# Performance work log

Hardware: AMD Instinct MI355X
Metric: run time of the kernel (lower is better)

The kernel has to match this reference:

```python
import jax, jax.numpy as jnp
import numpy as np

NUM_GROUPS = 32
EPS = 1e-6


def group_norm(x, scale, bias):
    # x: (b, c, t, h, w)
    b, c, t, h, w = x.shape
    xg = x.reshape(b, NUM_GROUPS, c // NUM_GROUPS, t, h, w)
    mean = jnp.mean(xg, axis=(2, 3, 4, 5), keepdims=True)
    var = jnp.var(xg, axis=(2, 3, 4, 5), keepdims=True)
    xg = (xg - mean) * jax.lax.rsqrt(var + EPS)
    xn = xg.reshape(b, c, t, h, w)
    return xn * scale[None, :, None, None, None] + bias[None, :, None, None, None]


def conv1x1(x, w, bvec):
    # 1x1x1 Conv3d == per-position linear over channels
    return jnp.einsum('oc,bcthw->bothw', w, x) + bvec[None, :, None, None, None]


def setup_inputs() -> dict:
    key = jax.random.key(0)
    ks = jax.random.split(key, 11)
    b, c, t, h, w = 2, 256, 4, 32, 32
    x = jax.random.normal(ks[0], (b, c, t, h, w), dtype=jnp.float32)
    s = 1.0 / np.sqrt(c)
    return {
        'x': x,
        'gn_scale': jnp.ones((c,), jnp.float32),
        'gn_bias': jnp.zeros((c,), jnp.float32),
        'wq': jax.random.normal(ks[1], (c, c), jnp.float32) * s,
        'bq': jax.random.normal(ks[2], (c,), jnp.float32) * 0.01,
        'wk': jax.random.normal(ks[3], (c, c), jnp.float32) * s,
        'bk': jax.random.normal(ks[4], (c,), jnp.float32) * 0.01,
        'wv': jax.random.normal(ks[5], (c, c), jnp.float32) * s,
        'bv': jax.random.normal(ks[6], (c,), jnp.float32) * 0.01,
        'wp': jax.random.normal(ks[7], (c, c), jnp.float32) * s,
        'bp': jax.random.normal(ks[8], (c,), jnp.float32) * 0.01,
    }


def reference(x, gn_scale, gn_bias, wq, bq, wk, bk, wv, bv, wp, bp):
    b, c, t, h, w = x.shape
    n = t * h * w
    h_ = group_norm(x, gn_scale, gn_bias)
    q = conv1x1(h_, wq, bq).reshape(b, c, n)  # (b, c, n)
    k = conv1x1(h_, wk, bk).reshape(b, c, n)
    v = conv1x1(h_, wv, bv).reshape(b, c, n)
    scale = jnp.asarray(int(c) ** (-0.5), x.dtype)
    # attn[b, i, j] = sum_c q[b,c,i] k[b,c,j]
    attn = jnp.einsum('bci,bcj->bij', q, k) * scale
    attn = jax.nn.softmax(attn, axis=2)
    # A[b, c, i] = sum_j v[b,c,j] attn[b,i,j]
    A = jnp.einsum('bcj,bij->bci', v, attn).reshape(b, c, t, h, w)
    A = conv1x1(A, wp, bp)
    return x + A
```

## Files before the change

### kernel.cpp

```cpp
#include <hip/hip_runtime.h>
#include <hip/hip_bf16.h>
#include <math.h>

#define BB 2
#define CC 256
#define GG 32
#define NN 4096
#define EPSF 1e-6f
#define JSPLIT 8
#define JBLK (NN / JSPLIT)
#define CH 32
#define NT (JBLK / CH)
#define QTILE 128
#define LOG2E 1.4426950408889634f

typedef _Float16 f16x8 __attribute__((ext_vector_type(8)));
typedef float f32x4 __attribute__((ext_vector_type(4)));
typedef float f32x16 __attribute__((ext_vector_type(16)));

static __device__ __forceinline__ unsigned short f2h_bits(float f) {
    _Float16 h = (_Float16)f;
    return __builtin_bit_cast(unsigned short, h);
}
static __device__ __forceinline__ unsigned pkh2(float a, float b) {
    return __builtin_bit_cast(unsigned, __builtin_amdgcn_cvt_pkrtz(a, b));
}
static __device__ __forceinline__ void gload16(const void* g, void* l) {
    __builtin_amdgcn_global_load_lds(
        (const __attribute__((address_space(1))) void*)g,
        (__attribute__((address_space(3))) void*)l, 16, 0, 0);
}

__global__ __launch_bounds__(256) void prep_w16_kernel(
    const float* __restrict__ wq, const float* __restrict__ wk,
    const float* __restrict__ wv, const float* __restrict__ wp,
    unsigned short* __restrict__ w16)
{
    int m = blockIdx.y;
    const float* src = (m == 0) ? wq : (m == 1) ? wk : (m == 2) ? wv : wp;
    float scale = (m == 0) ? 0.0625f * LOG2E : 1.0f;
    int idx = blockIdx.x * 256 + threadIdx.x;
    float4 v = ((const float4*)src)[idx];
    union { _Float16 h[4]; uint2 u; } pk;
    pk.h[0] = (_Float16)(v.x * scale);
    pk.h[1] = (_Float16)(v.y * scale);
    pk.h[2] = (_Float16)(v.z * scale);
    pk.h[3] = (_Float16)(v.w * scale);
    *(uint2*)(w16 + (size_t)m * CC * CC + (size_t)idx * 4) = pk.u;
}

__global__ __launch_bounds__(256) void gn_part_kernel(
    const float* __restrict__ x, float2* __restrict__ part)
{
    int g = blockIdx.x, p = blockIdx.y, b = blockIdx.z;
    const float* base = x + ((size_t)b * CC + (size_t)g * 8) * NN + (size_t)p * 8192;
    int t = threadIdx.x;
    float s = 0.f, ss = 0.f;
    for (int idx = t; idx < 2048; idx += 256) {
        float4 v4 = ((const float4*)base)[idx];
        s  += v4.x + v4.y + v4.z + v4.w;
        ss += v4.x*v4.x + v4.y*v4.y + v4.z*v4.z + v4.w*v4.w;
    }
    for (int off = 32; off; off >>= 1) {
        s  += __shfl_down(s,  off);
        ss += __shfl_down(ss, off);
    }
    __shared__ float red[8];
    int wid = t >> 6;
    if ((t & 63) == 0) { red[wid*2] = s; red[wid*2+1] = ss; }
    __syncthreads();
    if (t == 0) {
        part[(b*GG + g)*4 + p] = make_float2(red[0]+red[2]+red[4]+red[6],
                                             red[1]+red[3]+red[5]+red[7]);
    }
}

__global__ __launch_bounds__(256) void proj_qkv_kernel(
    const float* __restrict__ x, const float* __restrict__ sc,
    const float* __restrict__ bi, const float2* __restrict__ part,
    const unsigned short* __restrict__ w16,
    const float* __restrict__ bq, const float* __restrict__ bk,
    const float* __restrict__ bv,
    unsigned short* __restrict__ qT, unsigned short* __restrict__ kT,
    unsigned short* __restrict__ vC)
{
    int b  = blockIdx.y;
    int i0 = blockIdx.x * 32;
    int t  = threadIdx.x;
    __shared__ unsigned short htile[32 * 256];
    __shared__ float s_mean[GG], s_rstd[GG], s_sc[CC], s_bi[CC];
    if (t < GG) {
        float2 p0 = part[(b*GG + t)*4 + 0];
        float2 p1 = part[(b*GG + t)*4 + 1];
        float2 p2 = part[(b*GG + t)*4 + 2];
        float2 p3 = part[(b*GG + t)*4 + 3];
        float S  = p0.x + p1.x + p2.x + p3.x;
        float SS = p0.y + p1.y + p2.y + p3.y;
        float mean = S / 32768.f;
        float var  = SS / 32768.f - mean * mean;
        s_mean[t] = mean;
        s_rstd[t] = rsqrtf(var + EPSF);
    }
    s_sc[t] = sc[t];
    s_bi[t] = bi[t];
    __syncthreads();

    char* hw = (char*)htile;
    int nq = (t & 7) * 4;
    int cq = (t >> 3) * 4;
    #pragma unroll
    for (int k = 0; k < 2; k++) {
        int c0 = cq + k * 128;
        float4 xr[4];
        float aa[4], dd[4];
        #pragma unroll
        for (int e = 0; e < 4; e++) {
            int c = c0 + e;
            xr[e] = *(const float4*)(x + ((size_t)b*CC + c)*NN + i0 + nq);
            aa[e] = s_rstd[c >> 3] * s_sc[c];
            dd[e] = s_bi[c] - s_mean[c >> 3] * aa[e];
        }
        #pragma unroll
        for (int j = 0; j < 4; j++) {
            int row = nq + j;
            union { _Float16 h[4]; uint2 u; } pk;
            pk.h[0] = (_Float16)(((const float*)&xr[0])[j] * aa[0] + dd[0]);
            pk.h[1] = (_Float16)(((const float*)&xr[1])[j] * aa[1] + dd[1]);
            pk.h[2] = (_Float16)(((const float*)&xr[2])[j] * aa[2] + dd[2]);
            pk.h[3] = (_Float16)(((const float*)&xr[3])[j] * aa[3] + dd[3]);
            int off = row*512 + (((c0 >> 3) ^ (row & 7)) << 4) + (c0 & 7) * 2;
            *(uint2*)(hw + off) = pk.u;
        }
    }
    __syncthreads();

    int lane = t & 63, w = t >> 6;
    int col = lane & 15, grp = lane >> 4;
    const char* hr = (const char*)htile;

    #pragma unroll
    for (int p = 0; p < 2; p++) {
        const unsigned short* wgt = w16 + (size_t)p * CC * CC;
        const float* bias = p ? bk : bq;
        unsigned short* outp = (p ? kT : qT) + (size_t)b * NN * CC;
        float osc = p ? 1.0f : 0.0625f * LOG2E;
        #pragma unroll
        for (int ot = 0; ot < 4; ot++) {
            int ow = ot * 64 + w * 16;
            f32x4 acc[2];
            acc[0] = (f32x4){0.f,0.f,0.f,0.f};
            acc[1] = (f32x4){0.f,0.f,0.f,0.f};
            #pragma unroll
            for (int ck = 0; ck < 8; ck++) {
                f16x8 af = *(const f16x8*)(wgt + (size_t)(ow + col)*CC + ck*32 + grp*8);
                #pragma unroll
                for (int it = 0; it < 2; it++) {
                    int row = it*16 + col;
                    f16x8 bf = *(const f16x8*)(hr + row*512 + (((ck*4 + grp) ^ (row & 7)) << 4));
                    acc[it] = __builtin_amdgcn_mfma_f32_16x16x32_f16(af, bf, acc[it], 0, 0, 0);
                }
            }
            int obase = ow + grp * 4;
            float b0 = bias[obase]*osc, b1 = bias[obase+1]*osc,
                  b2 = bias[obase+2]*osc, b3 = bias[obase+3]*osc;
            #pragma unroll
            for (int it = 0; it < 2; it++) {
                int i = i0 + it*16 + col;
                union { _Float16 h[4]; uint2 u; } pk;
                pk.h[0] = (_Float16)(acc[it][0] + b0);
                pk.h[1] = (_Float16)(acc[it][1] + b1);
                pk.h[2] = (_Float16)(acc[it][2] + b2);
                pk.h[3] = (_Float16)(acc[it][3] + b3);
                *(uint2*)(outp + (size_t)i*CC + obase) = pk.u;
            }
        }
    }
    {
        const unsigned short* wgt = w16 + (size_t)2 * CC * CC;
        unsigned short* outp = vC + (size_t)b * CC * NN;
        int ibase = (w & 1) * 16;
        #pragma unroll
        for (int gg = 0; gg < 2; gg++) {
            int og = (w >> 1) * 2 + gg;
            f32x4 acc[4];
            #pragma unroll
            for (int ot = 0; ot < 4; ot++) acc[ot] = (f32x4){0.f,0.f,0.f,0.f};
            #pragma unroll
            for (int ck = 0; ck < 8; ck++) {
                int row = ibase + col;
                f16x8 af = *(const f16x8*)(hr + row*512 + (((ck*4 + grp) ^ (row & 7)) << 4));
                #pragma unroll
                for (int ot = 0; ot < 4; ot++) {
                    f16x8 bf = *(const f16x8*)(wgt + (size_t)(og*64 + ot*16 + col)*CC + ck*32 + grp*8);
                    acc[ot] = __builtin_amdgcn_mfma_f32_16x16x32_f16(af, bf, acc[ot], 0, 0, 0);
                }
            }
            int iw = i0 + ibase + grp * 4;
            #pragma unroll
            for (int ot = 0; ot < 4; ot++) {
                int o = og*64 + ot*16 + col;
                float bo = bv[o];
                union { _Float16 h[4]; uint2 u; } pk;
                pk.h[0] = (_Float16)(acc[ot][0] + bo);
                pk.h[1] = (_Float16)(acc[ot][1] + bo);
                pk.h[2] = (_Float16)(acc[ot][2] + bo);
                pk.h[3] = (_Float16)(acc[ot][3] + bo);
                *(uint2*)(outp + (size_t)o*NN + iw) = pk.u;
            }
        }
    }
}

#define STAGE_K(tt, bb) do { int _j = jlo + (tt)*CH; _Pragma("unroll") \
    for (int e = 0; e < 4; e++) gload16(kb + (size_t)_j*CC + koff[e], &bufK[bb][(4*w + e)*512]); } while (0)
#define STAGE_V(tt, bb) do { int _j = jlo + (tt)*CH; _Pragma("unroll") \
    for (int e = 0; e < 4; e++) gload16(vb + voff[e] + _j, &bufV[bb][(4*w + e)*512]); } while (0)

__global__ __launch_bounds__(256, 2) void attn_kernel(
    const unsigned short* __restrict__ qT,
    const unsigned short* __restrict__ kT,
    const unsigned short* __restrict__ vC,
    unsigned short* __restrict__ pO,
    float2* __restrict__ ml)
{
    int qt = blockIdx.x, s = blockIdx.y, b = blockIdx.z;
    int tid = threadIdx.x, w = tid >> 6, lane = tid & 63;
    int l31 = lane & 31, hi = lane >> 5;
    int col = lane & 15, grp = lane >> 4;
    int q0 = qt * QTILE + w * 32;
    int jlo = s * JBLK;

    __shared__ __align__(16) unsigned short bufK[2][8192];
    __shared__ __align__(16) unsigned short bufV[2][8192];
    __shared__ __align__(16) unsigned short plds[4 * 1280];

    const unsigned short* qb = qT + (size_t)b * NN * CC;
    const unsigned short* kb = kT + (size_t)b * NN * CC;
    const unsigned short* vb = vC + (size_t)b * CC * NN;

    f16x8 qf[16];
    #pragma unroll
    for (int ck = 0; ck < 16; ck++)
        qf[ck] = *(const f16x8*)(qb + (size_t)(q0 + l31)*CC + ck*16 + hi*8);

    int koff[4], voff[4];
    #pragma unroll
    for (int e = 0; e < 4; e++) {
        int blk = (4*w + e)*64 + lane;
        int kj = blk >> 5, kcb = blk & 31;
        koff[e] = kj*CC + ((kcb ^ (kj & 7)) * 8);
        int vc = blk >> 2, vcb = blk & 3;
        voff[e] = vc*NN + ((vcb ^ ((vc >> 1) & 3)) * 8);
    }
    int kru = l31 * 512;
    int kx  = l31 & 7;
    int vrb = col*64 + ((grp ^ ((col >> 1) & 3)) << 4);
    char* pw  = (char*)plds + w*2560 + l31*80 + 8*hi;
    const char* prd = (const char*)plds + w*2560;

    f32x4 O0[16], O1[16];
    #pragma unroll
    for (int ct = 0; ct < 16; ct++) {
        O0[ct] = (f32x4){0.f,0.f,0.f,0.f};
        O1[ct] = (f32x4){0.f,0.f,0.f,0.f};
    }
    float m = -1e30f, l = 0.f;

    STAGE_K(0, 0);
    STAGE_V(0, 0);
    __syncthreads();

    for (int t = 0; t < NT; t++) {
        int cur = t & 1;
        if (t + 1 < NT) {
            STAGE_K(t + 1, cur ^ 1);
            STAGE_V(t + 1, cur ^ 1);
        }
        const char* kbase = (const char*)&bufK[cur][0];
        const char* vbase = (const char*)&bufV[cur][0];

        f32x16 S;
        #pragma unroll
        for (int r = 0; r < 16; r++) S[r] = 0.f;
        __builtin_amdgcn_s_setprio(1);
        #pragma unroll
        for (int ck = 0; ck < 16; ck++) {
            f16x8 kf = *(const f16x8*)(kbase + kru + ((((ck*2) | hi) ^ kx) << 4));
            S = __builtin_amdgcn_mfma_f32_32x32x16_f16(kf, qf[ck], S, 0, 0, 0);
        }
        __builtin_amdgcn_s_setprio(0);

        float x0 = fmaxf(fmaxf(S[0], S[1]), fmaxf(S[2], S[3]));
        float x1 = fmaxf(fmaxf(S[4], S[5]), fmaxf(S[6], S[7]));
        float x2 = fmaxf(fmaxf(S[8], S[9]), fmaxf(S[10], S[11]));
        float x3 = fmaxf(fmaxf(S[12], S[13]), fmaxf(S[14], S[15]));
        float mh = fmaxf(fmaxf(x0, x1), fmaxf(x2, x3));
        float mx = fmaxf(mh, __shfl_xor(mh, 32));

        if (!__all(mx <= m + 8.f)) {
            float mn = fmaxf(m, mx);
            float f = exp2f(m - mn);
            m = mn;
            l *= f;
            float fq0 = __shfl(f, col);
            float fq1 = __shfl(f, 16 + col);
            #pragma unroll
            for (int ct = 0; ct < 16; ct++) { O0[ct] *= fq0; O1[ct] *= fq1; }
        }

        #pragma unroll
        for (int r = 0; r < 16; r++) S[r] = exp2f(S[r] - m);
        float ps = (((S[0]+S[1]) + (S[2]+S[3])) + ((S[4]+S[5]) + (S[6]+S[7])))
                 + (((S[8]+S[9]) + (S[10]+S[11])) + ((S[12]+S[13]) + (S[14]+S[15])));
        l += ps + __shfl_xor(ps, 32);

        {
            unsigned* pr = (unsigned*)pw;
            pr[0]  = pkh2(S[0],  S[1]);   pr[1]  = pkh2(S[2],  S[3]);
            pr[4]  = pkh2(S[4],  S[5]);   pr[5]  = pkh2(S[6],  S[7]);
            pr[8]  = pkh2(S[8],  S[9]);   pr[9]  = pkh2(S[10], S[11]);
            pr[12] = pkh2(S[12], S[13]);  pr[13] = pkh2(S[14], S[15]);
        }
        asm volatile("s_waitcnt lgkmcnt(0)" ::: "memory");
        __builtin_amdgcn_sched_barrier(0);

        f16x8 y0 = *(const f16x8*)(prd + col*80 + grp*16);
        f16x8 y1 = *(const f16x8*)(prd + (16 + col)*80 + grp*16);
        __builtin_amdgcn_s_setprio(1);
        #pragma unroll
        for (int ct = 0; ct < 16; ct++) {
            f16x8 xf = *(const f16x8*)(vbase + ct*1024 + vrb);
            O0[ct] = __builtin_amdgcn_mfma_f32_16x16x32_f16(xf, y0, O0[ct], 0, 0, 0);
            O1[ct] = __builtin_amdgcn_mfma_f32_16x16x32_f16(xf, y1, O1[ct], 0, 0, 0);
        }
        __builtin_amdgcn_s_setprio(0);
        __syncthreads();
    }

    float inv = 1.f / l;
    float iq0 = __shfl(inv, col);
    float iq1 = __shfl(inv, 16 + col);
    unsigned short* po = pO + ((size_t)(s*BB + b)*NN + q0) * CC;
    #pragma unroll
    for (int ct = 0; ct < 16; ct++) {
        int c = ct*16 + grp*4;
        *(unsigned*)(po + (size_t)col*CC + c)            = pkh2(O0[ct][0]*iq0, O0[ct][1]*iq0);
        *(unsigned*)(po + (size_t)col*CC + c + 2)        = pkh2(O0[ct][2]*iq0, O0[ct][3]*iq0);
        *(unsigned*)(po + (size_t)(16 + col)*CC + c)     = pkh2(O1[ct][0]*iq1, O1[ct][1]*iq1);
        *(unsigned*)(po + (size_t)(16 + col)*CC + c + 2) = pkh2(O1[ct][2]*iq1, O1[ct][3]*iq1);
    }
    if (lane < 32)
        ml[(size_t)(s*BB + b)*NN + q0 + lane] = make_float2(m, l);
}

__global__ __launch_bounds__(256) void attn_merge_kernel(
    const unsigned short* __restrict__ pO, const float2* __restrict__ ml,
    unsigned short* __restrict__ aT)
{
    int t = threadIdx.x;
    int qrow = blockIdx.x * 16 + (t >> 4);
    int c0 = (t & 15) * 16;
    float M = -1e30f;
    float m8[JSPLIT], l8[JSPLIT];
    #pragma unroll
    for (int s = 0; s < JSPLIT; s++) {
        float2 v = ml[(size_t)s*BB*NN + qrow];
        m8[s] = v.x; l8[s] = v.y;
        M = fmaxf(M, v.x);
    }
    float W = 0.f, wt[JSPLIT];
    #pragma unroll
    for (int s = 0; s < JSPLIT; s++) { wt[s] = l8[s] * exp2f(m8[s] - M); W += wt[s]; }
    float iW = 1.f / W;
    float acc[16];
    #pragma unroll
    for (int e = 0; e < 16; e++) acc[e] = 0.f;
    #pragma unroll
    for (int s = 0; s < JSPLIT; s++) {
        const unsigned short* p = pO + ((size_t)s*BB*NN + qrow)*CC + c0;
        f16x8 a0 = *(const f16x8*)p;
        f16x8 a1 = *(const f16x8*)(p + 8);
        float ws = wt[s] * iW;
        #pragma unroll
        for (int e = 0; e < 8; e++) {
            acc[e]     += ws * (float)a0[e];
            acc[e + 8] += ws * (float)a1[e];
        }
    }
    union { _Float16 h[8]; uint4 u; } o0, o1;
    #pragma unroll
    for (int e = 0; e < 8; e++) { o0.h[e] = (_Float16)acc[e]; o1.h[e] = (_Float16)acc[e+8]; }
    unsigned short* dst = aT + (size_t)qrow*CC + c0;
    *(uint4*)dst = o0.u;
    *(uint4*)(dst + 8) = o1.u;
}

__global__ __launch_bounds__(256) void proj_out_kernel(
    const unsigned short* __restrict__ aT,
    const unsigned short* __restrict__ wp16, const float* __restrict__ bp,
    const float* __restrict__ x, float* __restrict__ out)
{
    int b = blockIdx.z;
    int i0 = blockIdx.x * 64, o0 = blockIdx.y * 64;
    int lane = threadIdx.x & 63, wid = threadIdx.x >> 6;
    int col = lane & 15, grp = lane >> 4;
    int ibase = i0 + wid * 16;
    const unsigned short* ab = aT + (size_t)b*NN*CC;
    f32x4 acc[4];
    for (int ot = 0; ot < 4; ot++) acc[ot] = (f32x4){0.f,0.f,0.f,0.f};
    for (int ck = 0; ck < 8; ck++) {
        f16x8 af = *(const f16x8*)(ab + (size_t)(ibase + col)*CC + ck*32 + grp*8);
        for (int ot = 0; ot < 4; ot++) {
            f16x8 bf = *(const f16x8*)(wp16 + (size_t)(o0 + ot*16 + col)*CC + ck*32 + grp*8);
            acc[ot] = __builtin_amdgcn_mfma_f32_16x16x32_f16(af, bf, acc[ot], 0, 0, 0);
        }
    }
    int iw = ibase + grp * 4;
    for (int ot = 0; ot < 4; ot++) {
        int o = o0 + ot*16 + col;
        float bo = bp[o];
        size_t base = (size_t)b*CC*NN + (size_t)o*NN + iw;
        float4 x4 = *(const float4*)(x + base);
        float4 r;
        r.x = x4.x + acc[ot][0] + bo;
        r.y = x4.y + acc[ot][1] + bo;
        r.z = x4.z + acc[ot][2] + bo;
        r.w = x4.w + acc[ot][3] + bo;
        *(float4*)(out + base) = r;
    }
}

extern "C" void kernel_launch(void* const* d_in, const int* in_sizes, int n_in,
                              void* d_out, int out_size, void* d_ws, size_t ws_size,
                              hipStream_t stream) {
    const float* x  = (const float*)d_in[0];
    const float* gs = (const float*)d_in[1];
    const float* gb = (const float*)d_in[2];
    const float* wq = (const float*)d_in[3];
    const float* bq = (const float*)d_in[4];
    const float* wk = (const float*)d_in[5];
    const float* bk = (const float*)d_in[6];
    const float* wv = (const float*)d_in[7];
    const float* bv = (const float*)d_in[8];
    const float* wp = (const float*)d_in[9];
    const float* bp = (const float*)d_in[10];
    float* out = (float*)d_out;

    char* ws = (char*)d_ws;
    const size_t sz = (size_t)BB * NN * CC * sizeof(unsigned short);
    unsigned short* qT  = (unsigned short*)(ws + sz);
    unsigned short* kT  = (unsigned short*)(ws + 2*sz);
    unsigned short* vC  = (unsigned short*)(ws + 3*sz);
    unsigned short* aT  = (unsigned short*)(ws + 4*sz);
    unsigned short* w16 = (unsigned short*)(ws + 5*sz);
    float2* part        = (float2*)(ws + 5*sz + 512*1024);
    float2* ml          = (float2*)(ws + 5*sz + 768*1024);
    unsigned short* pO  = (unsigned short*)(ws + 5*sz + 1280*1024);

    prep_w16_kernel<<<dim3(CC*CC/4/256, 4), 256, 0, stream>>>(wq, wk, wv, wp, w16);
    gn_part_kernel<<<dim3(GG, 4, BB), 256, 0, stream>>>(x, part);
    proj_qkv_kernel<<<dim3(NN/32, BB), 256, 0, stream>>>(x, gs, gb, part, w16,
                                                         bq, bk, bv, qT, kT, vC);
    attn_kernel<<<dim3(NN/QTILE, JSPLIT, BB), 256, 0, stream>>>(qT, kT, vC, pO, ml);
    attn_merge_kernel<<<dim3(BB*NN/16), 256, 0, stream>>>(pO, ml, aT);
    proj_out_kernel<<<dim3(NN/64, CC/64, BB), 256, 0, stream>>>(aT, w16 + 3*CC*CC, bp, x, out);
}
```

Before: 125.0 us.

## Read K and V tiles directly from global memory instead of LDS staging

Removes the double-buffered global-to-LDS staging of K and V tiles and the per-iteration block barrier, so each wave loads its K and V MFMA fragments straight from global memory (relying on L1/L2 for reuse across waves). This cuts LDS usage, which may allow higher occupancy, and removes the synchronisation. In exchange, every wave issues redundant global loads for the same tiles, with strided V accesses and no prefetch overlap, which risks exposing memory latency inside the MFMA loops.

Result: slower. 196.7 us (+57.4%).

```diff
diff --git a/kernel.cpp b/kernel.cpp
--- a/kernel.cpp
+++ b/kernel.cpp
@@ -24,11 +24,6 @@
 }
 static __device__ __forceinline__ unsigned pkh2(float a, float b) {
     return __builtin_bit_cast(unsigned, __builtin_amdgcn_cvt_pkrtz(a, b));
-}
-static __device__ __forceinline__ void gload16(const void* g, void* l) {
-    __builtin_amdgcn_global_load_lds(
-        (const __attribute__((address_space(1))) void*)g,
-        (__attribute__((address_space(3))) void*)l, 16, 0, 0);
 }
 
 __global__ __launch_bounds__(256) void prep_w16_kernel(
@@ -211,11 +206,6 @@
     }
 }
 
-#define STAGE_K(tt, bb) do { int _j = jlo + (tt)*CH; _Pragma("unroll") \
-    for (int e = 0; e < 4; e++) gload16(kb + (size_t)_j*CC + koff[e], &bufK[bb][(4*w + e)*512]); } while (0)
-#define STAGE_V(tt, bb) do { int _j = jlo + (tt)*CH; _Pragma("unroll") \
-    for (int e = 0; e < 4; e++) gload16(vb + voff[e] + _j, &bufV[bb][(4*w + e)*512]); } while (0)
-
 __global__ __launch_bounds__(256, 2) void attn_kernel(
     const unsigned short* __restrict__ qT,
     const unsigned short* __restrict__ kT,
@@ -230,8 +220,6 @@
     int q0 = qt * QTILE + w * 32;
     int jlo = s * JBLK;
 
-    __shared__ __align__(16) unsigned short bufK[2][8192];
-    __shared__ __align__(16) unsigned short bufV[2][8192];
     __shared__ __align__(16) unsigned short plds[4 * 1280];
 
     const unsigned short* qb = qT + (size_t)b * NN * CC;
@@ -243,18 +231,9 @@
     for (int ck = 0; ck < 16; ck++)
         qf[ck] = *(const f16x8*)(qb + (size_t)(q0 + l31)*CC + ck*16 + hi*8);
 
-    int koff[4], voff[4];
-    #pragma unroll
-    for (int e = 0; e < 4; e++) {
-        int blk = (4*w + e)*64 + lane;
-        int kj = blk >> 5, kcb = blk & 31;
-        koff[e] = kj*CC + ((kcb ^ (kj & 7)) * 8);
-        int vc = blk >> 2, vcb = blk & 3;
-        voff[e] = vc*NN + ((vcb ^ ((vc >> 1) & 3)) * 8);
-    }
-    int kru = l31 * 512;
-    int kx  = l31 & 7;
-    int vrb = col*64 + ((grp ^ ((col >> 1) & 3)) << 4);
+    const unsigned short* krow = kb + (size_t)(jlo + l31)*CC + hi*8;
+    const unsigned short* vrow = vb + (size_t)col*NN + jlo + grp*8;
+
     char* pw  = (char*)plds + w*2560 + l31*80 + 8*hi;
     const char* prd = (const char*)plds + w*2560;
 
@@ -266,26 +245,14 @@
     }
     float m = -1e30f, l = 0.f;
 
-    STAGE_K(0, 0);
-    STAGE_V(0, 0);
-    __syncthreads();
-
     for (int t = 0; t < NT; t++) {
-        int cur = t & 1;
-        if (t + 1 < NT) {
-            STAGE_K(t + 1, cur ^ 1);
-            STAGE_V(t + 1, cur ^ 1);
-        }
-        const char* kbase = (const char*)&bufK[cur][0];
-        const char* vbase = (const char*)&bufV[cur][0];
-
         f32x16 S;
         #pragma unroll
         for (int r = 0; r < 16; r++) S[r] = 0.f;
         __builtin_amdgcn_s_setprio(1);
         #pragma unroll
         for (int ck = 0; ck < 16; ck++) {
-            f16x8 kf = *(const f16x8*)(kbase + kru + ((((ck*2) | hi) ^ kx) << 4));
+            f16x8 kf = *(const f16x8*)(krow + ck*16);
             S = __builtin_amdgcn_mfma_f32_32x32x16_f16(kf, qf[ck], S, 0, 0, 0);
         }
         __builtin_amdgcn_s_setprio(0);
@@ -329,12 +296,14 @@
         __builtin_amdgcn_s_setprio(1);
         #pragma unroll
         for (int ct = 0; ct < 16; ct++) {
-            f16x8 xf = *(const f16x8*)(vbase + ct*1024 + vrb);
+            f16x8 xf = *(const f16x8*)(vrow + (size_t)(ct*16)*NN);
             O0[ct] = __builtin_amdgcn_mfma_f32_16x16x32_f16(xf, y0, O0[ct], 0, 0, 0);
             O1[ct] = __builtin_amdgcn_mfma_f32_16x16x32_f16(xf, y1, O1[ct], 0, 0, 0);
         }
         __builtin_amdgcn_s_setprio(0);
-        __syncthreads();
+
+        krow += (size_t)CH * CC;
+        vrow += CH;
     }
 
     float inv = 1.f / l;
```

## Fuse split-softmax merge into output projection and combine prep kernels

Applied to the files above, without the earlier changes.

Merges the weight fp16 conversion and group-norm partial-sum kernels into one launch by block-id dispatch. Fuses the attention split merge into the output projection: each block merges the JSPLIT partial outputs for 32 query rows into a swizzled LDS tile, then runs MFMA against Wp and adds the residual. This removes two launches and the aT round trip through global memory, at the cost of fewer, larger blocks in the final stage.

Result: faster. 116.9 us (median of 2 runs) (-6.4%).

```diff
diff --git a/kernel.cpp b/kernel.cpp
--- a/kernel.cpp
+++ b/kernel.cpp
@@ -12,6 +12,7 @@
 #define CH 32
 #define NT (JBLK / CH)
 #define QTILE 128
+#define ITILE 32
 #define LOG2E 1.4426950408889634f
 
 typedef _Float16 f16x8 __attribute__((ext_vector_type(8)));
@@ -31,47 +32,48 @@
         (__attribute__((address_space(3))) void*)l, 16, 0, 0);
 }
 
-__global__ __launch_bounds__(256) void prep_w16_kernel(
+__global__ __launch_bounds__(256) void prep_gn_kernel(
     const float* __restrict__ wq, const float* __restrict__ wk,
     const float* __restrict__ wv, const float* __restrict__ wp,
-    unsigned short* __restrict__ w16)
-{
-    int m = blockIdx.y;
-    const float* src = (m == 0) ? wq : (m == 1) ? wk : (m == 2) ? wv : wp;
-    float scale = (m == 0) ? 0.0625f * LOG2E : 1.0f;
-    int idx = blockIdx.x * 256 + threadIdx.x;
-    float4 v = ((const float4*)src)[idx];
-    union { _Float16 h[4]; uint2 u; } pk;
-    pk.h[0] = (_Float16)(v.x * scale);
-    pk.h[1] = (_Float16)(v.y * scale);
-    pk.h[2] = (_Float16)(v.z * scale);
-    pk.h[3] = (_Float16)(v.w * scale);
-    *(uint2*)(w16 + (size_t)m * CC * CC + (size_t)idx * 4) = pk.u;
-}
-
-__global__ __launch_bounds__(256) void gn_part_kernel(
+    unsigned short* __restrict__ w16,
     const float* __restrict__ x, float2* __restrict__ part)
 {
-    int g = blockIdx.x, p = blockIdx.y, b = blockIdx.z;
-    const float* base = x + ((size_t)b * CC + (size_t)g * 8) * NN + (size_t)p * 8192;
-    int t = threadIdx.x;
-    float s = 0.f, ss = 0.f;
-    for (int idx = t; idx < 2048; idx += 256) {
-        float4 v4 = ((const float4*)base)[idx];
-        s  += v4.x + v4.y + v4.z + v4.w;
-        ss += v4.x*v4.x + v4.y*v4.y + v4.z*v4.z + v4.w*v4.w;
-    }
-    for (int off = 32; off; off >>= 1) {
-        s  += __shfl_down(s,  off);
-        ss += __shfl_down(ss, off);
-    }
     __shared__ float red[8];
-    int wid = t >> 6;
-    if ((t & 63) == 0) { red[wid*2] = s; red[wid*2+1] = ss; }
-    __syncthreads();
-    if (t == 0) {
-        part[(b*GG + g)*4 + p] = make_float2(red[0]+red[2]+red[4]+red[6],
-                                             red[1]+red[3]+red[5]+red[7]);
+    int id = blockIdx.x;
+    int t  = threadIdx.x;
+    if (id < 256) {
+        int m = id >> 6;
+        const float* src = (m == 0) ? wq : (m == 1) ? wk : (m == 2) ? wv : wp;
+        float scale = (m == 0) ? 0.0625f * LOG2E : 1.0f;
+        int idx = (id & 63) * 256 + t;
+        float4 v = ((const float4*)src)[idx];
+        union { _Float16 h[4]; uint2 u; } pk;
+        pk.h[0] = (_Float16)(v.x * scale);
+        pk.h[1] = (_Float16)(v.y * scale);
+        pk.h[2] = (_Float16)(v.z * scale);
+        pk.h[3] = (_Float16)(v.w * scale);
+        *(uint2*)(w16 + (size_t)m * CC * CC + (size_t)idx * 4) = pk.u;
+    } else {
+        int rem = id - 256;
+        int g = rem & 31, p = (rem >> 5) & 3, b = rem >> 7;
+        const float* base = x + ((size_t)b * CC + (size_t)g * 8) * NN + (size_t)p * 8192;
+        float s = 0.f, ss = 0.f;
+        for (int idx = t; idx < 2048; idx += 256) {
+            float4 v4 = ((const float4*)base)[idx];
+            s  += v4.x + v4.y + v4.z + v4.w;
+            ss += v4.x*v4.x + v4.y*v4.y + v4.z*v4.z + v4.w*v4.w;
+        }
+        for (int off = 32; off; off >>= 1) {
+            s  += __shfl_down(s,  off);
+            ss += __shfl_down(ss, off);
+        }
+        int wid = t >> 6;
+        if ((t & 63) == 0) { red[wid*2] = s; red[wid*2+1] = ss; }
+        __syncthreads();
+        if (t == 0) {
+            part[(b*GG + g)*4 + p] = make_float2(red[0]+red[2]+red[4]+red[6],
+                                                 red[1]+red[3]+red[5]+red[7]);
+        }
     }
 }
 
@@ -353,80 +355,96 @@
         ml[(size_t)(s*BB + b)*NN + q0 + lane] = make_float2(m, l);
 }
 
-__global__ __launch_bounds__(256) void attn_merge_kernel(
+__global__ __launch_bounds__(256, 2) void proj_out_merge_kernel(
     const unsigned short* __restrict__ pO, const float2* __restrict__ ml,
-    unsigned short* __restrict__ aT)
-{
-    int t = threadIdx.x;
-    int qrow = blockIdx.x * 16 + (t >> 4);
-    int c0 = (t & 15) * 16;
-    float M = -1e30f;
-    float m8[JSPLIT], l8[JSPLIT];
-    #pragma unroll
-    for (int s = 0; s < JSPLIT; s++) {
-        float2 v = ml[(size_t)s*BB*NN + qrow];
-        m8[s] = v.x; l8[s] = v.y;
-        M = fmaxf(M, v.x);
-    }
-    float W = 0.f, wt[JSPLIT];
-    #pragma unroll
-    for (int s = 0; s < JSPLIT; s++) { wt[s] = l8[s] * exp2f(m8[s] - M); W += wt[s]; }
-    float iW = 1.f / W;
-    float acc[16];
-    #pragma unroll
-    for (int e = 0; e < 16; e++) acc[e] = 0.f;
-    #pragma unroll
-    for (int s = 0; s < JSPLIT; s++) {
-        const unsigned short* p = pO + ((size_t)s*BB*NN + qrow)*CC + c0;
-        f16x8 a0 = *(const f16x8*)p;
-        f16x8 a1 = *(const f16x8*)(p + 8);
-        float ws = wt[s] * iW;
-        #pragma unroll
-        for (int e = 0; e < 8; e++) {
-            acc[e]     += ws * (float)a0[e];
-            acc[e + 8] += ws * (float)a1[e];
-        }
-    }
-    union { _Float16 h[8]; uint4 u; } o0, o1;
-    #pragma unroll
-    for (int e = 0; e < 8; e++) { o0.h[e] = (_Float16)acc[e]; o1.h[e] = (_Float16)acc[e+8]; }
-    unsigned short* dst = aT + (size_t)qrow*CC + c0;
-    *(uint4*)dst = o0.u;
-    *(uint4*)(dst + 8) = o1.u;
-}
-
-__global__ __launch_bounds__(256) void proj_out_kernel(
-    const unsigned short* __restrict__ aT,
     const unsigned short* __restrict__ wp16, const float* __restrict__ bp,
     const float* __restrict__ x, float* __restrict__ out)
 {
-    int b = blockIdx.z;
-    int i0 = blockIdx.x * 64, o0 = blockIdx.y * 64;
-    int lane = threadIdx.x & 63, wid = threadIdx.x >> 6;
+    int b  = blockIdx.y;
+    int i0 = blockIdx.x * ITILE;
+    int t  = threadIdx.x;
+    __shared__ __align__(16) unsigned short htile[ITILE * 256];
+
+    {
+        int row  = t >> 3;
+        int cseg = (t & 7) * 32;
+        size_t qrow = (size_t)b * NN + i0 + row;
+        float M = -1e30f;
+        float m8[JSPLIT], l8[JSPLIT];
+        #pragma unroll
+        for (int s = 0; s < JSPLIT; s++) {
+            float2 v = ml[(size_t)s*BB*NN + qrow];
+            m8[s] = v.x; l8[s] = v.y;
+            M = fmaxf(M, v.x);
+        }
+        float W = 0.f, wt[JSPLIT];
+        #pragma unroll
+        for (int s = 0; s < JSPLIT; s++) { wt[s] = l8[s] * exp2f(m8[s] - M); W += wt[s]; }
+        float iW = 1.f / W;
+        float acc[32];
+        #pragma unroll
+        for (int e = 0; e < 32; e++) acc[e] = 0.f;
+        #pragma unroll
+        for (int s = 0; s < JSPLIT; s++) {
+            const unsigned short* p = pO + ((size_t)s*BB*NN + qrow)*CC + cseg;
+            float ws = wt[s] * iW;
+            #pragma unroll
+            for (int k = 0; k < 4; k++) {
+                f16x8 a = *(const f16x8*)(p + k*8);
+                #pragma unroll
+                for (int e = 0; e < 8; e++) acc[k*8 + e] += ws * (float)a[e];
+            }
+        }
+        char* hw = (char*)htile;
+        #pragma unroll
+        for (int k = 0; k < 4; k++) {
+            int c0 = cseg + k*8;
+            uint4 pk;
+            pk.x = pkh2(acc[k*8+0], acc[k*8+1]);
+            pk.y = pkh2(acc[k*8+2], acc[k*8+3]);
+            pk.z = pkh2(acc[k*8+4], acc[k*8+5]);
+            pk.w = pkh2(acc[k*8+6], acc[k*8+7]);
+            int off = row*512 + (((c0 >> 3) ^ (row & 7)) << 4);
+            *(uint4*)(hw + off) = pk;
+        }
+    }
+    __syncthreads();
+
+    int lane = t & 63, wid = t >> 6;
     int col = lane & 15, grp = lane >> 4;
-    int ibase = i0 + wid * 16;
-    const unsigned short* ab = aT + (size_t)b*NN*CC;
-    f32x4 acc[4];
-    for (int ot = 0; ot < 4; ot++) acc[ot] = (f32x4){0.f,0.f,0.f,0.f};
-    for (int ck = 0; ck < 8; ck++) {
-        f16x8 af = *(const f16x8*)(ab + (size_t)(ibase + col)*CC + ck*32 + grp*8);
+    int rl0 = (wid & 1) * 16;
+    int ibase = i0 + rl0;
+    const char* hr = (const char*)htile;
+    #pragma unroll
+    for (int gg = 0; gg < 2; gg++) {
+        int o0 = ((wid >> 1) * 2 + gg) * 64;
+        f32x4 acc[4];
+        #pragma unroll
+        for (int ot = 0; ot < 4; ot++) acc[ot] = (f32x4){0.f,0.f,0.f,0.f};
+        #pragma unroll
+        for (int ck = 0; ck < 8; ck++) {
+            int rl = rl0 + col;
+            f16x8 af = *(const f16x8*)(hr + rl*512 + (((ck*4 + grp) ^ (rl & 7)) << 4));
+            #pragma unroll
+            for (int ot = 0; ot < 4; ot++) {
+                f16x8 bf = *(const f16x8*)(wp16 + (size_t)(o0 + ot*16 + col)*CC + ck*32 + grp*8);
+                acc[ot] = __builtin_amdgcn_mfma_f32_16x16x32_f16(af, bf, acc[ot], 0, 0, 0);
+            }
+        }
+        int iw = ibase + grp * 4;
+        #pragma unroll
         for (int ot = 0; ot < 4; ot++) {
-            f16x8 bf = *(const f16x8*)(wp16 + (size_t)(o0 + ot*16 + col)*CC + ck*32 + grp*8);
-            acc[ot] = __builtin_amdgcn_mfma_f32_16x16x32_f16(af, bf, acc[ot], 0, 0, 0);
-        }
-    }
-    int iw = ibase + grp * 4;
-    for (int ot = 0; ot < 4; ot++) {
-        int o = o0 + ot*16 + col;
-        float bo = bp[o];
-        size_t base = (size_t)b*CC*NN + (size_t)o*NN + iw;
-        float4 x4 = *(const float4*)(x + base);
-        float4 r;
-        r.x = x4.x + acc[ot][0] + bo;
-        r.y = x4.y + acc[ot][1] + bo;
-        r.z = x4.z + acc[ot][2] + bo;
-        r.w = x4.w + acc[ot][3] + bo;
-        *(float4*)(out + base) = r;
+            int o = o0 + ot*16 + col;
+            float bo = bp[o];
+            size_t base = (size_t)b*CC*NN + (size_t)o*NN + iw;
+            float4 x4 = *(const float4*)(x + base);
+            float4 r;
+            r.x = x4.x + acc[ot][0] + bo;
+            r.y = x4.y + acc[ot][1] + bo;
+            r.z = x4.z + acc[ot][2] + bo;
+            r.w = x4.w + acc[ot][3] + bo;
+            *(float4*)(out + base) = r;
+        }
     }
 }
 
@@ -451,17 +469,15 @@
     unsigned short* qT  = (unsigned short*)(ws + sz);
     unsigned short* kT  = (unsigned short*)(ws + 2*sz);
     unsigned short* vC  = (unsigned short*)(ws + 3*sz);
-    unsigned short* aT  = (unsigned short*)(ws + 4*sz);
     unsigned short* w16 = (unsigned short*)(ws + 5*sz);
     float2* part        = (float2*)(ws + 5*sz + 512*1024);
     float2* ml          = (float2*)(ws + 5*sz + 768*1024);
     unsigned short* pO  = (unsigned short*)(ws + 5*sz + 1280*1024);
 
-    prep_w16_kernel<<<dim3(CC*CC/4/256, 4), 256, 0, stream>>>(wq, wk, wv, wp, w16);
-    gn_part_kernel<<<dim3(GG, 4, BB), 256, 0, stream>>>(x, part);
+    prep_gn_kernel<<<dim3(512), 256, 0, stream>>>(wq, wk, wv, wp, w16, x, part);
     proj_qkv_kernel<<<dim3(NN/32, BB), 256, 0, stream>>>(x, gs, gb, part, w16,
                                                          bq, bk, bv, qT, kT, vC);
     attn_kernel<<<dim3(NN/QTILE, JSPLIT, BB), 256, 0, stream>>>(qT, kT, vC, pO, ml);
-    attn_merge_kernel<<<dim3(BB*NN/16), 256, 0, stream>>>(pO, ml, aT);
-    proj_out_kernel<<<dim3(NN/64, CC/64, BB), 256, 0, stream>>>(aT, w16 + 3*CC*CC, bp, x, out);
-}
+    proj_out_merge_kernel<<<dim3(NN/ITILE, BB), 256, 0, stream>>>(pO, ml, w16 + 3*CC*CC,
+                                                                  bp, x, out);
+}
```
